# Kernel optimization log

Hardware: AMD Instinct MI355X
Metric: run time of the kernel (lower is better)

## Reference

```python
import jax, jax.numpy as jnp
import numpy as np

N_NODES = 50000
N_EDGES = 800000
IN_DIM = 256     # state_size
HID = 256        # hidden_dim
ACT = 64         # action_size


def gcn_conv(x, src, dst, norm, W, b):
    # PyG GCNConv: out[dst] += norm_e * (x @ W)[src]; then + bias
    h = x @ W                               # [N, out]
    msg = h[src] * norm[:, None]            # [E+N, out]
    agg = jax.ops.segment_sum(msg, dst, num_segments=N_NODES)
    return agg + b


def gcn_norm(edge_index):
    # add self-loops, symmetric normalization deg^-1/2[src]*deg^-1/2[dst]
    loops = jnp.arange(N_NODES, dtype=edge_index.dtype)
    src = jnp.concatenate([edge_index[0], loops])
    dst = jnp.concatenate([edge_index[1], loops])
    deg = jax.ops.segment_sum(jnp.ones_like(dst, dtype=jnp.float32), dst,
                              num_segments=N_NODES)
    dinv = jnp.where(deg > 0, jax.lax.rsqrt(deg), 0.0)
    norm = dinv[src] * dinv[dst]            # [E+N]
    return src, dst, norm


def setup_inputs() -> dict:
    key = jax.random.key(0)
    ks = jax.random.split(key, 12)
    x = jax.random.normal(ks[0], (N_NODES, IN_DIM), dtype=jnp.float32)
    edge_index = jax.random.randint(ks[1], (2, N_EDGES), 0, N_NODES, dtype=jnp.int64)

    def glorot(k, shape):
        lim = float(np.sqrt(6.0 / (shape[0] + shape[1])))
        return jax.random.uniform(k, shape, jnp.float32, -lim, lim)

    return {
        "x": x, "edge_index": edge_index,
        "W1": glorot(ks[2], (IN_DIM, HID)), "b1": jnp.zeros((HID,), jnp.float32),
        "W2": glorot(ks[3], (HID, HID)),    "b2": jnp.zeros((HID,), jnp.float32),
        "fcW1": glorot(ks[4], (HID, HID)),  "fcb1": jnp.zeros((HID,), jnp.float32),
        "fcW2": glorot(ks[5], (HID, HID)),  "fcb2": jnp.zeros((HID,), jnp.float32),
        "fcW3": glorot(ks[6], (HID, ACT)),  "fcb3": jnp.zeros((ACT,), jnp.float32),
    }


def reference(x, edge_index, W1, b1, W2, b2, fcW1, fcb1, fcW2, fcb2, fcW3, fcb3):
    src, dst, norm = gcn_norm(edge_index)
    h = jax.nn.relu(gcn_conv(x, src, dst, norm, W1, b1))   # GNNLayer 1
    h = jax.nn.relu(gcn_conv(h, src, dst, norm, W2, b2))   # GNNLayer 2
    g = jax.nn.relu(jnp.mean(h, axis=0)[None, :])          # [1, HID]
    g = jax.nn.relu(g @ fcW1 + fcb1)
    g = jax.nn.relu(g @ fcW2 + fcb2)
    return g @ fcW3 + fcb3                                 # [1, ACT]
```

## Files before the change

### kernel.cpp

```cpp
#include <hip/hip_runtime.h>

#define N_NODES 50000
#define N_EDGES 800000
#define DIM 256
#define ACT 64
#define SCAN_B 256
#define SCAN_NB ((N_NODES + SCAN_B - 1) / SCAN_B)
#define SLICE_ELEMS ((size_t)N_NODES * 32)
#define AGG_CHUNKS 512
#define TOTAL_GROUPS (AGG_CHUNKS * 32)
#define CSR_MAX (N_EDGES + 8 * N_NODES + 64)
#define NBINS 16
#define NBB (NBINS * SCAN_NB)

typedef __attribute__((ext_vector_type(8))) short short8_t;
typedef __attribute__((ext_vector_type(4))) float f32x4;
typedef __attribute__((ext_vector_type(4))) unsigned short ushort4_t;

__device__ __forceinline__ unsigned short f2b(float x) {
    unsigned u = __float_as_uint(x);
    unsigned r = u + 0x7FFFu + ((u >> 16) & 1u);
    return (unsigned short)(r >> 16);
}

__device__ __forceinline__ int deg_bin(int deg) {
    int rounds = ((deg + 8) & ~7) >> 3;
    return (rounds > NBINS - 1) ? NBINS - 1 : rounds;
}


__global__ __launch_bounds__(256) void k_cvt_wt2(const float* __restrict__ W1,
                                                 const float* __restrict__ W2,
                                                 unsigned short* __restrict__ W1t,
                                                 unsigned short* __restrict__ W2t) {
    int b = blockIdx.x;
    const float* W = (b < 256) ? W1 : W2;
    unsigned short* Wt = (b < 256) ? W1t : W2t;
    int i = (b & 255) * 256 + threadIdx.x;
    int k = i >> 8, n = i & 255;
    Wt[n * DIM + k] = f2b(W[k * DIM + n]);
}


__global__ void k_deg_count(const int* __restrict__ ei, int* degi) {
    int e = blockIdx.x * blockDim.x + threadIdx.x;
    if (e < N_EDGES) atomicAdd(&degi[ei[N_EDGES + e]], 1);
}


__global__ __launch_bounds__(256) void k_hist_rank(const int* __restrict__ degi,
                                                   int* blockbin,
                                                   unsigned char* lrank) {
    __shared__ int lh[NBINS];
    int t = threadIdx.x;
    if (t < NBINS) lh[t] = 0;
    __syncthreads();
    int i = blockIdx.x * 256 + t;
    if (i < N_NODES) {
        int bin = deg_bin(degi[i]);
        lrank[i] = (unsigned char)atomicAdd(&lh[bin], 1);
    }
    __syncthreads();
    if (t < NBINS) blockbin[t * SCAN_NB + blockIdx.x] = lh[t];
}

__global__ __launch_bounds__(256) void k_scan_bins(const int* __restrict__ blockbin,
                                                   int* blockbase) {
    __shared__ int sm[256];
    int t = threadIdx.x;
    const int CH = (NBB + 255) / 256;
    int s0 = t * CH;
    int s1 = s0 + CH; if (s1 > NBB) s1 = NBB;
    int s = 0;
    for (int i = s0; i < s1; ++i) s += blockbin[i];
    sm[t] = s;
    __syncthreads();
#pragma unroll
    for (int off = 1; off < 256; off <<= 1) {
        int u = (t >= off) ? sm[t - off] : 0;
        __syncthreads();
        sm[t] += u;
        __syncthreads();
    }
    int base = sm[t] - s;
    for (int i = s0; i < s1; ++i) { int v = blockbin[i]; blockbase[i] = base; base += v; }
}

__global__ __launch_bounds__(256) void k_perm_apply(const int* __restrict__ degi,
                                                    const int* __restrict__ blockbase,
                                                    const unsigned char* __restrict__ lrank,
                                                    int* perm) {
    int i = blockIdx.x * 256 + threadIdx.x;
    if (i >= N_NODES) return;
    int bin = deg_bin(degi[i]);
    perm[blockbase[bin * SCAN_NB + blockIdx.x] + lrank[i]] = i;
}


__global__ __launch_bounds__(SCAN_B) void k_scan_local(const int* __restrict__ degi,
                                                       int* lexc, int* btot) {
    __shared__ int sm[SCAN_B];
    int t = threadIdx.x;
    int i = blockIdx.x * SCAN_B + t;
    int v = (i < N_NODES) ? ((degi[i] + 8) & ~7) : 0;
    sm[t] = v;
    __syncthreads();
#pragma unroll
    for (int off = 1; off < SCAN_B; off <<= 1) {
        int u = (t >= off) ? sm[t - off] : 0;
        __syncthreads();
        sm[t] += u;
        __syncthreads();
    }
    if (i < N_NODES) lexc[i] = sm[t] - v;
    if (t == SCAN_B - 1) btot[blockIdx.x] = sm[t];
}

__global__ __launch_bounds__(SCAN_B) void k_scan_tops(const int* __restrict__ btot,
                                                      int* bbase, int* rowstart) {
    __shared__ int sm[SCAN_B];
    int t = threadIdx.x;
    int v = (t < SCAN_NB) ? btot[t] : 0;
    sm[t] = v;
    __syncthreads();
#pragma unroll
    for (int off = 1; off < SCAN_B; off <<= 1) {
        int u = (t >= off) ? sm[t - off] : 0;
        __syncthreads();
        sm[t] += u;
        __syncthreads();
    }
    if (t < SCAN_NB) bbase[t] = sm[t] - v;
    if (t == SCAN_NB - 1) rowstart[N_NODES] = sm[t];
}

__global__ __launch_bounds__(SCAN_B) void k_scan_apply(const int* __restrict__ degi,
                                                       const int* __restrict__ lexc,
                                                       const int* __restrict__ bbase,
                                                       int* rowstart, int* fillpos,
                                                       float* dinv, unsigned* csr4) {
    int i = blockIdx.x * SCAN_B + threadIdx.x;
    if (i >= N_NODES) return;
    int rs = bbase[blockIdx.x] + lexc[i];
    rowstart[i] = rs;
    int d = degi[i] + 1;
    float di = rsqrtf((float)d);
    dinv[i] = di;
    csr4[rs] = ((unsigned)i << 16) | f2b(di * di);
    fillpos[i] = rs + 1;
}

__global__ void k_fill_edge(const int* __restrict__ ei,
                            const float* __restrict__ dinv, int* fillpos,
                            unsigned* csr4) {
    int e = blockIdx.x * blockDim.x + threadIdx.x;
    if (e < N_EDGES) {
        int s = ei[e];
        int d = ei[N_EDGES + e];
        int p = atomicAdd(&fillpos[d], 1);
        csr4[p] = ((unsigned)s << 16) | f2b(dinv[s] * dinv[d]);
    }
}


template <int AFP32>
__global__ __launch_bounds__(512) void k_gemm_mfma(const void* __restrict__ Ap,
                                                   const unsigned short* __restrict__ Wt,
                                                   unsigned short* __restrict__ H,
                                                   int M) {
    __shared__ char lds[49152];
    char* AsB = lds;
    char* BsB = lds + 16384;

    int tid = threadIdx.x;
    int w = tid >> 6;
    int l = tid & 63;
    int wr = w >> 2, wc = w & 3;
    int r0 = blockIdx.x * 128;

    f32x4 acc[4][4];
#pragma unroll
    for (int i = 0; i < 4; ++i)
#pragma unroll
        for (int j = 0; j < 4; ++j) acc[i][j] = (f32x4)(0.f);

    for (int kt = 0; kt < 4; ++kt) {
        int k0 = kt * 64;
#pragma unroll
        for (int i = 0; i < 2; ++i) {
            int c = tid + i * 512;
            int row = c >> 3, kc = c & 7;
            int gg = r0 + row; if (gg >= M) gg = M - 1;
            short8_t v;
            if (AFP32) {
                const float* A = (const float*)Ap;
                const float4* src = (const float4*)(A + (size_t)gg * DIM + k0 + kc * 8);
                float4 f0 = src[0], f1 = src[1];
                v[0] = (short)f2b(f0.x); v[1] = (short)f2b(f0.y);
                v[2] = (short)f2b(f0.z); v[3] = (short)f2b(f0.w);
                v[4] = (short)f2b(f1.x); v[5] = (short)f2b(f1.y);
                v[6] = (short)f2b(f1.z); v[7] = (short)f2b(f1.w);
            } else {
                const unsigned short* A = (const unsigned short*)Ap;
                int k = k0 + kc * 8;
                int slice = k >> 5, within = k & 31;
                v = *(const short8_t*)(A + (size_t)slice * SLICE_ELEMS + (size_t)gg * 32 + within);
            }
            int off = (row * 128 + kc * 16) ^ ((row & 7) << 4);
            *(short8_t*)(AsB + off) = v;
        }
#pragma unroll
        for (int i = 0; i < 4; ++i) {
            int c = tid + i * 512;
            int n = c >> 3, kc = c & 7;
            short8_t v = *(const short8_t*)(Wt + n * DIM + k0 + kc * 8);
            int off = (n * 128 + kc * 16) ^ ((n & 7) << 4);
            *(short8_t*)(BsB + off) = v;
        }
        __syncthreads();

#pragma unroll
        for (int kf = 0; kf < 2; ++kf) {
            int kb = kf * 64 + (l >> 4) * 16;
            short8_t a[4], b[4];
#pragma unroll
            for (int fm = 0; fm < 4; ++fm) {
                int ra = wr * 64 + fm * 16 + (l & 15);
                a[fm] = *(const short8_t*)(AsB + ((ra * 128 + kb) ^ ((ra & 7) << 4)));
            }
#pragma unroll
            for (int fn = 0; fn < 4; ++fn) {
                int nb = wc * 64 + fn * 16 + (l & 15);
                b[fn] = *(const short8_t*)(BsB + ((nb * 128 + kb) ^ ((nb & 7) << 4)));
            }
#pragma unroll
            for (int fm = 0; fm < 4; ++fm)
#pragma unroll
                for (int fn = 0; fn < 4; ++fn)
                    acc[fm][fn] = __builtin_amdgcn_mfma_f32_16x16x32_bf16(
                        a[fm], b[fn], acc[fm][fn], 0, 0, 0);
        }
        __syncthreads();
    }

#pragma unroll
    for (int fm = 0; fm < 4; ++fm) {
#pragma unroll
        for (int i = 0; i < 4; ++i) {
            int row = r0 + wr * 64 + fm * 16 + ((l >> 4) << 2) + i;
            if (row >= M) continue;
#pragma unroll
            for (int fn = 0; fn < 4; ++fn) {
                int col = wc * 64 + fn * 16 + (l & 15);
                int slice = col >> 5;
                H[(size_t)slice * SLICE_ELEMS + (size_t)row * 32 + (col & 31)] = f2b(acc[fm][fn][i]);
            }
        }
    }
}


__global__ __launch_bounds__(256) void k_agg_sliced(const unsigned short* __restrict__ H,
                                                    const int* __restrict__ rowstart,
                                                    const unsigned* __restrict__ csr4,
                                                    const int* __restrict__ perm,
                                                    const float* __restrict__ bias,
                                                    unsigned short* __restrict__ X,
                                                    float* __restrict__ gsum,
                                                    int write_out) {
    __shared__ unsigned pbuf[32 * 68];
    int slice = blockIdx.x & 7;
    int chunk = blockIdx.x >> 3;
    int g = threadIdx.x >> 3;
    int lane = threadIdx.x & 7;
    const char* Hb = (const char*)(H + (size_t)slice * SLICE_ELEMS) + (lane << 3);
    unsigned short* Xs = X + (size_t)slice * SLICE_ELEMS;
    int d0 = slice * 32 + lane * 4;
    float4 bb = *(const float4*)&bias[d0];
    float c0 = 0.f, c1 = 0.f, c2 = 0.f, c3 = 0.f;
    unsigned* ps = pbuf + g * 68;
    int fg = chunk * 32 + g;
    for (int idx = fg; idx < N_NODES; idx += TOTAL_GROUPS) {
        int n = perm[idx];
        int beg = rowstart[n], end = rowstart[n + 1];
        float a0 = 0.f, a1 = 0.f, a2 = 0.f, a3 = 0.f;
        uint4 u = *(const uint4*)(csr4 + beg + (lane << 2));
        int r = 0;
        for (int e = beg; e < end; e += 32, ++r) {
            int en = (e + 32 < end) ? e + 32 : e;
            uint4 un = *(const uint4*)(csr4 + en + (lane << 2));
            unsigned* pb = ps + (r & 1) * 32;
            *(uint4*)(pb + (lane << 2)) = u;
#pragma unroll
            for (int s = 0; s < 4; ++s) {
                if (e + (s << 3) >= end) break;
#pragma unroll
                for (int i = 0; i < 8; ++i) {
                    unsigned p = pb[(s << 3) + i];
                    unsigned off = (p >> 16) << 6;
                    float nm = __uint_as_float(p << 16);
                    uint2 q = *(const uint2*)(Hb + off);
                    a0 = fmaf(nm, __uint_as_float(q.x << 16), a0);
                    a1 = fmaf(nm, __uint_as_float(q.x & 0xFFFF0000u), a1);
                    a2 = fmaf(nm, __uint_as_float(q.y << 16), a2);
                    a3 = fmaf(nm, __uint_as_float(q.y & 0xFFFF0000u), a3);
                }
            }
            u = un;
        }
        float o0 = fmaxf(a0 + bb.x, 0.f);
        float o1 = fmaxf(a1 + bb.y, 0.f);
        float o2 = fmaxf(a2 + bb.z, 0.f);
        float o3 = fmaxf(a3 + bb.w, 0.f);
        if (write_out) {
            ushort4_t o; o.x = f2b(o0); o.y = f2b(o1); o.z = f2b(o2); o.w = f2b(o3);
            *(ushort4_t*)(Xs + (size_t)n * 32 + (lane << 2)) = o;
        }
        c0 += o0; c1 += o1; c2 += o2; c3 += o3;
    }
    if (gsum) {
        __shared__ float4 smr[256];
        int tid = threadIdx.x;
        smr[tid] = make_float4(c0, c1, c2, c3);
        __syncthreads();
#pragma unroll
        for (int off = 128; off >= 8; off >>= 1) {
            if (tid < off) {
                float4 a = smr[tid], b = smr[tid + off];
                smr[tid] = make_float4(a.x + b.x, a.y + b.y, a.z + b.z, a.w + b.w);
            }
            __syncthreads();
        }
        if (tid < 8) {
            float4 v = smr[tid];
            atomicAdd(&gsum[d0], v.x);
            atomicAdd(&gsum[d0 + 1], v.y);
            atomicAdd(&gsum[d0 + 2], v.z);
            atomicAdd(&gsum[d0 + 3], v.w);
        }
    }
}


__global__ __launch_bounds__(256) void k_fc(const float* __restrict__ gsum,
                                            const float* __restrict__ fcW1,
                                            const float* __restrict__ fcb1,
                                            const float* __restrict__ fcW2,
                                            const float* __restrict__ fcb2,
                                            const float* __restrict__ fcW3,
                                            const float* __restrict__ fcb3,
                                            float* __restrict__ out) {
    __shared__ float g[DIM];
    __shared__ float h[DIM];
    int t = threadIdx.x;
    g[t] = fmaxf(gsum[t] * (1.0f / (float)N_NODES), 0.f);
    __syncthreads();
    float acc = fcb1[t];
    for (int k = 0; k < DIM; ++k) acc = fmaf(g[k], fcW1[k * DIM + t], acc);
    h[t] = fmaxf(acc, 0.f);
    __syncthreads();
    acc = fcb2[t];
    for (int k = 0; k < DIM; ++k) acc = fmaf(h[k], fcW2[k * DIM + t], acc);
    __syncthreads();
    g[t] = fmaxf(acc, 0.f);
    __syncthreads();
    if (t < ACT) {
        float o = fcb3[t];
        for (int k = 0; k < DIM; ++k) o = fmaf(g[k], fcW3[k * ACT + t], o);
        out[t] = o;
    }
}


extern "C" void kernel_launch(void* const* d_in, const int* in_sizes, int n_in,
                              void* d_out, int out_size, void* d_ws, size_t ws_size,
                              hipStream_t stream) {
    const float* x    = (const float*)d_in[0];
    const int*   ei   = (const int*)d_in[1];
    const float* W1   = (const float*)d_in[2];
    const float* b1   = (const float*)d_in[3];
    const float* W2   = (const float*)d_in[4];
    const float* b2   = (const float*)d_in[5];
    const float* fcW1 = (const float*)d_in[6];
    const float* fcb1 = (const float*)d_in[7];
    const float* fcW2 = (const float*)d_in[8];
    const float* fcb2 = (const float*)d_in[9];
    const float* fcW3 = (const float*)d_in[10];
    const float* fcb3 = (const float*)d_in[11];
    float* out = (float*)d_out;

    char* w = (char*)d_ws;
    size_t o = 0;
#define CARVE(name, type, count) \
    type* name = (type*)(w + o); \
    o += (((size_t)(count) * sizeof(type)) + 255) & ~(size_t)255;
    CARVE(degi, int, N_NODES)
    CARVE(rowstart, int, N_NODES + 1)
    CARVE(fillpos, int, N_NODES)
    CARVE(dinv, float, N_NODES)
    CARVE(lexc, int, N_NODES)
    CARVE(btot, int, SCAN_NB)
    CARVE(bbase, int, SCAN_NB)
    CARVE(blockbin, int, NBB)
    CARVE(blockbase, int, NBB)
    CARVE(perm, int, N_NODES)
    CARVE(lrank, unsigned char, N_NODES)
    CARVE(csr4, unsigned, CSR_MAX)
    CARVE(gsum, float, DIM)
    CARVE(W1t, unsigned short, DIM * DIM)
    CARVE(W2t, unsigned short, DIM * DIM)
    CARVE(Hbuf, unsigned short, (size_t)N_NODES * DIM)
    CARVE(Xbuf, unsigned short, (size_t)N_NODES * DIM)
#undef CARVE

    hipMemsetAsync(gsum, 0, DIM * sizeof(float), stream);
    hipMemsetAsync(degi, 0, N_NODES * sizeof(int), stream);
    hipMemsetAsync(csr4, 0, (size_t)CSR_MAX * sizeof(unsigned), stream);

    k_cvt_wt2<<<512, 256, 0, stream>>>(W1, W2, W1t, W2t);

    k_deg_count<<<(N_EDGES + 255) / 256, 256, 0, stream>>>(ei, degi);
    k_hist_rank<<<SCAN_NB, 256, 0, stream>>>(degi, blockbin, lrank);
    k_scan_bins<<<1, 256, 0, stream>>>(blockbin, blockbase);
    k_perm_apply<<<SCAN_NB, 256, 0, stream>>>(degi, blockbase, lrank, perm);
    k_scan_local<<<SCAN_NB, SCAN_B, 0, stream>>>(degi, lexc, btot);
    k_scan_tops<<<1, SCAN_B, 0, stream>>>(btot, bbase, rowstart);
    k_scan_apply<<<SCAN_NB, SCAN_B, 0, stream>>>(degi, lexc, bbase, rowstart, fillpos,
                                                 dinv, csr4);
    k_fill_edge<<<(N_EDGES + 255) / 256, 256, 0, stream>>>(ei, dinv, fillpos, csr4);

    int gemm_grid = (N_NODES + 127) / 128;
    k_gemm_mfma<1><<<gemm_grid, 512, 0, stream>>>(x, W1t, Hbuf, N_NODES);
    k_agg_sliced<<<8 * AGG_CHUNKS, 256, 0, stream>>>(Hbuf, rowstart, csr4, perm, b1,
                                                     Xbuf, (float*)nullptr, 1);
    k_gemm_mfma<0><<<gemm_grid, 512, 0, stream>>>(Xbuf, W2t, Hbuf, N_NODES);
    k_agg_sliced<<<8 * AGG_CHUNKS, 256, 0, stream>>>(Hbuf, rowstart, csr4, perm, b2,
                                                     Xbuf, gsum, 0);

    k_fc<<<1, 256, 0, stream>>>(gsum, fcW1, fcb1, fcW2, fcb2, fcW3, fcb3, out);
}
```

Measured before the change: 281.5 us.

## Order CSR rows by permuted index, pad rows to 16, batch 16 gathers

CSR rows are now laid out in permutation order, so each aggregation group reads rowstart and its edge list at contiguous positions, and the degree-to-node lookup goes through perm. Row padding and degree bins move from multiples of 8 to multiples of 16. The inner gather loop now issues 16 independent H loads before the FMAs, to expose more memory-level parallelism. In exchange the padded CSR grows and more padded zero-weight entries get processed, and register pressure rises from the 16-wide load arrays.

```diff
diff --git a/kernel.cpp b/kernel.cpp
--- a/kernel.cpp
+++ b/kernel.cpp
@@ -9,7 +9,7 @@
 #define SLICE_ELEMS ((size_t)N_NODES * 32)
 #define AGG_CHUNKS 512
 #define TOTAL_GROUPS (AGG_CHUNKS * 32)
-#define CSR_MAX (N_EDGES + 8 * N_NODES + 64)
+#define CSR_MAX (N_EDGES + 16 * N_NODES + 64)
 #define NBINS 16
 #define NBB (NBINS * SCAN_NB)
 
@@ -24,7 +24,7 @@
 }
 
 __device__ __forceinline__ int deg_bin(int deg) {
-    int rounds = ((deg + 8) & ~7) >> 3;
+    int rounds = ((deg + 16) & ~15) >> 4;
     return (rounds > NBINS - 1) ? NBINS - 1 : rounds;
 }
 
@@ -98,11 +98,12 @@
 
 
 __global__ __launch_bounds__(SCAN_B) void k_scan_local(const int* __restrict__ degi,
+                                                       const int* __restrict__ perm,
                                                        int* lexc, int* btot) {
     __shared__ int sm[SCAN_B];
     int t = threadIdx.x;
     int i = blockIdx.x * SCAN_B + t;
-    int v = (i < N_NODES) ? ((degi[i] + 8) & ~7) : 0;
+    int v = (i < N_NODES) ? ((degi[perm[i]] + 16) & ~15) : 0;
     sm[t] = v;
     __syncthreads();
 #pragma unroll
@@ -135,6 +136,7 @@
 }
 
 __global__ __launch_bounds__(SCAN_B) void k_scan_apply(const int* __restrict__ degi,
+                                                       const int* __restrict__ perm,
                                                        const int* __restrict__ lexc,
                                                        const int* __restrict__ bbase,
                                                        int* rowstart, int* fillpos,
@@ -143,11 +145,12 @@
     if (i >= N_NODES) return;
     int rs = bbase[blockIdx.x] + lexc[i];
     rowstart[i] = rs;
-    int d = degi[i] + 1;
+    int n = perm[i];
+    int d = degi[n] + 1;
     float di = rsqrtf((float)d);
-    dinv[i] = di;
-    csr4[rs] = ((unsigned)i << 16) | f2b(di * di);
-    fillpos[i] = rs + 1;
+    dinv[n] = di;
+    csr4[rs] = ((unsigned)n << 16) | f2b(di * di);
+    fillpos[n] = rs + 1;
 }
 
 __global__ void k_fill_edge(const int* __restrict__ ei,
@@ -282,7 +285,7 @@
     int fg = chunk * 32 + g;
     for (int idx = fg; idx < N_NODES; idx += TOTAL_GROUPS) {
         int n = perm[idx];
-        int beg = rowstart[n], end = rowstart[n + 1];
+        int beg = rowstart[idx], end = rowstart[idx + 1];
         float a0 = 0.f, a1 = 0.f, a2 = 0.f, a3 = 0.f;
         uint4 u = *(const uint4*)(csr4 + beg + (lane << 2));
         int r = 0;
@@ -292,18 +295,22 @@
             unsigned* pb = ps + (r & 1) * 32;
             *(uint4*)(pb + (lane << 2)) = u;
 #pragma unroll
-            for (int s = 0; s < 4; ++s) {
-                if (e + (s << 3) >= end) break;
-#pragma unroll
-                for (int i = 0; i < 8; ++i) {
-                    unsigned p = pb[(s << 3) + i];
-                    unsigned off = (p >> 16) << 6;
-                    float nm = __uint_as_float(p << 16);
-                    uint2 q = *(const uint2*)(Hb + off);
-                    a0 = fmaf(nm, __uint_as_float(q.x << 16), a0);
-                    a1 = fmaf(nm, __uint_as_float(q.x & 0xFFFF0000u), a1);
-                    a2 = fmaf(nm, __uint_as_float(q.y << 16), a2);
-                    a3 = fmaf(nm, __uint_as_float(q.y & 0xFFFF0000u), a3);
+            for (int s = 0; s < 2; ++s) {
+                if (e + (s << 4) >= end) break;
+                unsigned pp[16];
+#pragma unroll
+                for (int i = 0; i < 16; ++i) pp[i] = pb[(s << 4) + i];
+                uint2 q[16];
+#pragma unroll
+                for (int i = 0; i < 16; ++i)
+                    q[i] = *(const uint2*)(Hb + ((pp[i] >> 16) << 6));
+#pragma unroll
+                for (int i = 0; i < 16; ++i) {
+                    float nm = __uint_as_float(pp[i] << 16);
+                    a0 = fmaf(nm, __uint_as_float(q[i].x << 16), a0);
+                    a1 = fmaf(nm, __uint_as_float(q[i].x & 0xFFFF0000u), a1);
+                    a2 = fmaf(nm, __uint_as_float(q[i].y << 16), a2);
+                    a3 = fmaf(nm, __uint_as_float(q[i].y & 0xFFFF0000u), a3);
                 }
             }
             u = un;
@@ -423,10 +430,10 @@
     k_hist_rank<<<SCAN_NB, 256, 0, stream>>>(degi, blockbin, lrank);
     k_scan_bins<<<1, 256, 0, stream>>>(blockbin, blockbase);
     k_perm_apply<<<SCAN_NB, 256, 0, stream>>>(degi, blockbase, lrank, perm);
-    k_scan_local<<<SCAN_NB, SCAN_B, 0, stream>>>(degi, lexc, btot);
+    k_scan_local<<<SCAN_NB, SCAN_B, 0, stream>>>(degi, perm, lexc, btot);
     k_scan_tops<<<1, SCAN_B, 0, stream>>>(btot, bbase, rowstart);
-    k_scan_apply<<<SCAN_NB, SCAN_B, 0, stream>>>(degi, lexc, bbase, rowstart, fillpos,
-                                                 dinv, csr4);
+    k_scan_apply<<<SCAN_NB, SCAN_B, 0, stream>>>(degi, perm, lexc, bbase, rowstart,
+                                                 fillpos, dinv, csr4);
     k_fill_edge<<<(N_EDGES + 255) / 256, 256, 0, stream>>>(ei, dinv, fillpos, csr4);
 
     int gemm_grid = (N_NODES + 127) / 128;
```

After: 281.4 us. About the same (-0.0%).
